# Kernel tuning notes

Measured on AMD Instinct MI355X. Metric: run time of the kernel, lower is better.

The kernel has to match this reference:

```python
import jax, jax.numpy as jnp
import numpy as np
import math

PHI = (1 + math.sqrt(5)) / 2
TABLE_SIZE = 4096
TWO_PI = 2.0 * math.pi
_ang = np.arange(TABLE_SIZE, dtype=np.float32) * (TWO_PI / TABLE_SIZE)
SIN_T = jnp.asarray(np.sin(_ang))
COS_T = jnp.asarray(np.cos(_ang))


def lookup_sin_cos(theta):
    """LUT sin/cos with linear interpolation over a 4096-entry table on [0, 2pi)."""
    pos = (theta / TWO_PI % 1.0) * TABLE_SIZE
    i0f = jnp.floor(pos)
    frac = pos - i0f
    i0 = i0f.astype(jnp.int32) % TABLE_SIZE
    i1 = (i0 + 1) % TABLE_SIZE
    s = SIN_T[i0] * (1.0 - frac) + SIN_T[i1] * frac
    c = COS_T[i0] * (1.0 - frac) + COS_T[i1] * frac
    return s, c


def setup_inputs() -> dict:
    key = jax.random.key(0)
    ks = jax.random.split(key, 8)
    B, S, D, H = 2, 2048, 1024, 16
    dh = D // H
    return {
        "x": jax.random.normal(ks[0], (B, S, D), dtype=jnp.float32),
        "w_q": jax.random.normal(ks[1], (H, dh), dtype=jnp.float32) * 0.02,
        "b_q": jnp.zeros((H, dh), jnp.float32),
        "phi_q": jnp.full((H, dh), PHI, jnp.float32),
        "w_k": jax.random.normal(ks[2], (H, dh), dtype=jnp.float32) * 0.02,
        "b_k": jnp.zeros((H, dh), jnp.float32),
        "phi_k": jnp.full((H, dh), PHI, jnp.float32),
        "w_v": jax.random.normal(ks[3], (H, dh), dtype=jnp.float32) * 0.02,
        "b_v": jnp.zeros((H, dh), jnp.float32),
        "w_out": jax.random.normal(ks[4], (D,), dtype=jnp.float32) * 0.02,
        "b_out": jnp.zeros((D,), jnp.float32),
    }


def reference(x, w_q, b_q, phi_q, w_k, b_k, phi_k, w_v, b_v, w_out, b_out):
    B, S, D = x.shape
    H, dh = w_q.shape
    scale = math.sqrt(2 * dh)
    t = jnp.arange(S, dtype=x.dtype).reshape(1, S, 1, 1)
    xh = x.reshape(B, S, H, dh)

    theta_q = xh / (1.0 + jnp.abs(w_q)) + b_q + t * phi_q
    sin_q, cos_q = lookup_sin_cos(theta_q)
    Q = jnp.concatenate([cos_q, sin_q], axis=-1)  # (B,S,H,2dh)

    theta_k = xh / (1.0 + jnp.abs(w_k)) + b_k + t * phi_k
    sin_k, cos_k = lookup_sin_cos(theta_k)
    K = jnp.concatenate([cos_k, sin_k], axis=-1)  # (B,S,H,2dh)

    theta_v = xh / (1.0 + jnp.abs(w_v)) + b_v
    sin_v, cos_v = lookup_sin_cos(theta_v)
    V = cos_v + sin_v  # (B,S,H,dh)

    scores = jnp.einsum('bqhd,bkhd->bhqk', Q, K) / scale
    causal = jnp.triu(jnp.ones((S, S), dtype=bool), k=1)
    scores = jnp.where(causal, -jnp.inf, scores)
    attn = jax.nn.softmax(scores, axis=-1)
    out = jnp.einsum('bhqk,bkhd->bqhd', attn, V).reshape(B, S, D)

    theta_out = out / (1.0 + jnp.abs(w_out)) + b_out
    sin_o, cos_o = lookup_sin_cos(theta_out)
    return cos_o + sin_o
```

## Files before the change

kernel.cpp:

```cpp
#include <hip/hip_runtime.h>
#include <hip/hip_bf16.h>
#include <math.h>

#define BB 2
#define SS 2048
#define HH 16
#define DH 64
#define DQK 128
#define DD (HH*DH)
#define QS2   0.12751758f
#define EBIAS 11.5415605f

typedef _Float16 half8_t __attribute__((ext_vector_type(8)));
typedef _Float16 half4_t __attribute__((ext_vector_type(4)));
typedef float f32x4_t __attribute__((ext_vector_type(4)));
typedef float f32x4v __attribute__((ext_vector_type(4)));

__device__ __forceinline__ void fsincos(float th, float* sn, float* cs) {
  float rev = th * 0.15915494309189535f;
  rev -= floorf(rev);
#if __has_builtin(__builtin_amdgcn_sinf) && __has_builtin(__builtin_amdgcn_cosf)
  *sn = __builtin_amdgcn_sinf(rev);
  *cs = __builtin_amdgcn_cosf(rev);
#else
  float ang = rev * 6.283185307179586f;
  *sn = __sinf(ang);
  *cs = __cosf(ang);
#endif
}

__device__ __forceinline__ float frcp(float v) {
#if __has_builtin(__builtin_amdgcn_rcpf)
  return __builtin_amdgcn_rcpf(v);
#else
  return 1.f / v;
#endif
}

__device__ __forceinline__ void dma16(const void* g, void* l) {
  __builtin_amdgcn_global_load_lds(
      (const __attribute__((address_space(1))) unsigned int*)g,
      (__attribute__((address_space(3))) unsigned int*)l, 16, 0, 0);
}

__global__ __launch_bounds__(256) void gen_qkv(
    const float* __restrict__ x,
    const float* __restrict__ wq, const float* __restrict__ bq,
    const float* __restrict__ phq,
    const float* __restrict__ wk, const float* __restrict__ bk,
    const float* __restrict__ phk,
    const float* __restrict__ wv, const float* __restrict__ bv,
    _Float16* __restrict__ Qd, _Float16* __restrict__ Kd, _Float16* __restrict__ Vtd)
{
  int stile = blockIdx.x >> 5;
  int bh    = blockIdx.x & 31;
  int b = bh >> 4, h = bh & 15;
  int t = threadIdx.x;
  int sl = t >> 2;
  int dq = (t & 3) << 4;
  int s  = stile * 64 + sl;

  __shared__ _Float16 Vl[64 * 65];

  const float* xr = x + (((size_t)b * SS + s) * HH + h) * DH + dq;
  float tv = (float)s;
  int hd0 = h * DH + dq;
  _Float16 qc[16], qs[16], kc[16], ks[16];
#pragma unroll
  for (int g = 0; g < 4; g++) {
    f32x4v x4  = *(const f32x4v*)(xr + g * 4);
    f32x4v wq4 = *(const f32x4v*)(wq + hd0 + g * 4);
    f32x4v bq4 = *(const f32x4v*)(bq + hd0 + g * 4);
    f32x4v pq4 = *(const f32x4v*)(phq + hd0 + g * 4);
    f32x4v wk4 = *(const f32x4v*)(wk + hd0 + g * 4);
    f32x4v bk4 = *(const f32x4v*)(bk + hd0 + g * 4);
    f32x4v pk4 = *(const f32x4v*)(phk + hd0 + g * 4);
    f32x4v wv4 = *(const f32x4v*)(wv + hd0 + g * 4);
    f32x4v bv4 = *(const f32x4v*)(bv + hd0 + g * 4);
#pragma unroll
    for (int i2 = 0; i2 < 4; i2++) {
      int i = g * 4 + i2;
      float xv = x4[i2];
      {
        float th = xv * frcp(1.f + fabsf(wq4[i2])) + fmaf(tv, pq4[i2], bq4[i2]);
        float sn, cs; fsincos(th, &sn, &cs);
        qc[i] = (_Float16)(cs * QS2);
        qs[i] = (_Float16)(sn * QS2);
      }
      {
        float th = xv * frcp(1.f + fabsf(wk4[i2])) + fmaf(tv, pk4[i2], bk4[i2]);
        float sn, cs; fsincos(th, &sn, &cs);
        kc[i] = (_Float16)cs;
        ks[i] = (_Float16)sn;
      }
      {
        float th = xv * frcp(1.f + fabsf(wv4[i2])) + bv4[i2];
        float sn, cs; fsincos(th, &sn, &cs);
        Vl[(dq + i) * 65 + sl] = (_Float16)(cs + sn);
      }
    }
  }
  size_t qbase = ((size_t)bh * SS + s) * DQK;
#pragma unroll
  for (int i = 0; i < 2; i++) {
    *(half8_t*)(Qd + qbase + dq + i * 8)      = *(half8_t*)(&qc[i * 8]);
    *(half8_t*)(Qd + qbase + DH + dq + i * 8) = *(half8_t*)(&qs[i * 8]);
  }
  {
    size_t ktb = ((size_t)bh * 32 + stile) * 8192;
    int fo0 = (t & 3) * 2;
    *(half8_t*)(Kd + ktb + ((size_t)(fo0    ) * 64 + sl) * 8) = *(half8_t*)(&kc[0]);
    *(half8_t*)(Kd + ktb + ((size_t)(fo0 + 1) * 64 + sl) * 8) = *(half8_t*)(&kc[8]);
    *(half8_t*)(Kd + ktb + ((size_t)(fo0 + 8) * 64 + sl) * 8) = *(half8_t*)(&ks[0]);
    *(half8_t*)(Kd + ktb + ((size_t)(fo0 + 9) * 64 + sl) * 8) = *(half8_t*)(&ks[8]);
  }
  __syncthreads();
#pragma unroll
  for (int i = 0; i < 2; i++) {
    int u = t * 2 + i;
    int dv = u & 63, ku = u >> 6;
    _Float16 tmp[8];
#pragma unroll
    for (int jj = 0; jj < 8; jj++) tmp[jj] = Vl[dv * 65 + ku * 8 + jj];
    *(half8_t*)(Vtd + (((size_t)bh * 32 + stile) * 8 + ku) * 512 + dv * 8) =
        *(half8_t*)tmp;
  }
}

__global__ __launch_bounds__(256) void flash_attn(
    const _Float16* __restrict__ Qd, const _Float16* __restrict__ Kd,
    const _Float16* __restrict__ Vtd,
    const float* __restrict__ wout, const float* __restrict__ bout,
    float* __restrict__ out)
{
  int qt = 31 - (blockIdx.x >> 5);
  int bh = blockIdx.x & 31;
  int b  = bh >> 4, hh = bh & 15;
  int nch = qt + 1;
  int q0 = qt * 64;
  int wave = threadIdx.x >> 6;
  int lane = threadIdx.x & 63;
  int lm = lane & 15, lq = lane >> 4;
  int qh = wave >> 1;
  int kh = wave & 1;

  __shared__ __align__(16) _Float16 KB[2][8192];

  const _Float16* Kg = Kd + (size_t)bh * 32 * 8192;
  const _Float16* Vg = Vtd + (size_t)bh * 32 * 4096;

  {
#pragma unroll
    for (int i = 0; i < 4; i++)
      dma16(Kg + (size_t)(wave * 4 + i) * 512 + lane * 8, &KB[0][(wave * 4 + i) * 512]);
  }

  const _Float16* Qb = Qd + ((size_t)bh * SS + q0 + qh * 32) * DQK;
  half8_t aq[2][4];
#pragma unroll
  for (int qtl = 0; qtl < 2; qtl++)
#pragma unroll
    for (int c = 0; c < 4; c++)
      aq[qtl][c] = *(const half8_t*)(Qb + (qtl * 16 + lm) * DQK + c * 32 + lq * 8);

  f32x4_t o[4][2];
  float l[2] = {0.f, 0.f};
#pragma unroll
  for (int dt = 0; dt < 4; dt++)
#pragma unroll
    for (int qtl = 0; qtl < 2; qtl++) o[dt][qtl] = (f32x4_t){0.f, 0.f, 0.f, 0.f};

  const f32x4_t cinit = (f32x4_t){-EBIAS, -EBIAS, -EBIAS, -EBIAS};

  const _Float16* Vw = Vg + ((size_t)(lq >> 1) * 64 + lm) * 8 + (lq & 1) * 4 +
                       (size_t)kh * 4 * 64 * 8;

  for (int kt = 0; kt < nch; ++kt) {
    int bf = kt & 1;
    __syncthreads();

    half4_t vr[4][2];
    {
      const _Float16* vsrc = Vw + (size_t)kt * 4096;
#pragma unroll
      for (int dt = 0; dt < 4; dt++)
#pragma unroll
        for (int kg = 0; kg < 2; kg++)
          vr[dt][kg] = *(const half4_t*)(vsrc + ((size_t)kg * 2 * 64 + dt * 16) * 8);
    }

    if (kt + 1 < nch) {
      int nb = (kt + 1) & 1;
      const _Float16* gK = Kg + (size_t)(kt + 1) * 8192;
#pragma unroll
      for (int i = 0; i < 4; i++)
        dma16(gK + (size_t)(wave * 4 + i) * 512 + lane * 8, &KB[nb][(wave * 4 + i) * 512]);
    }

    const _Float16* lK = &KB[bf][0];
    int k0 = kt * 64;

    f32x4_t cST[2][2];
    cST[0][0] = cST[0][1] = cST[1][0] = cST[1][1] = cinit;
#pragma unroll
    for (int c = 0; c < 4; c++) {
      half8_t k0f = *(const half8_t*)(lK + ((size_t)(c * 4 + lq) * 64 + kh * 32 + lm) * 8);
      half8_t k1f = *(const half8_t*)(lK + ((size_t)(c * 4 + lq) * 64 + kh * 32 + 16 + lm) * 8);
      cST[0][0] = __builtin_amdgcn_mfma_f32_16x16x32_f16(k0f, aq[0][c], cST[0][0], 0, 0, 0);
      cST[0][1] = __builtin_amdgcn_mfma_f32_16x16x32_f16(k0f, aq[1][c], cST[0][1], 0, 0, 0);
      cST[1][0] = __builtin_amdgcn_mfma_f32_16x16x32_f16(k1f, aq[0][c], cST[1][0], 0, 0, 0);
      cST[1][1] = __builtin_amdgcn_mfma_f32_16x16x32_f16(k1f, aq[1][c], cST[1][1], 0, 0, 0);
    }

    bool maskit = (kt == nch - 1);
    half4_t pb[2][2];
#pragma unroll
    for (int ktl = 0; ktl < 2; ktl++)
#pragma unroll
      for (int qtl = 0; qtl < 2; qtl++) {
        float pf[4];
#pragma unroll
        for (int r = 0; r < 4; r++) {
          float sv = cST[ktl][qtl][r];
          if (maskit) {
            int key  = k0 + kh * 32 + ktl * 16 + lq * 4 + r;
            int qrow = q0 + qh * 32 + qtl * 16 + lm;
            if (key > qrow) sv = -1e30f;
          }
          pf[r] = __builtin_exp2f(sv);
          l[qtl] += pf[r];
        }
        pb[ktl][qtl] = (half4_t){(_Float16)pf[0], (_Float16)pf[1],
                                 (_Float16)pf[2], (_Float16)pf[3]};
      }

#pragma unroll
    for (int dt = 0; dt < 4; dt++)
#pragma unroll
      for (int kg = 0; kg < 2; kg++) {
        o[dt][0] = __builtin_amdgcn_mfma_f32_16x16x16f16(vr[dt][kg], pb[kg][0], o[dt][0], 0, 0, 0);
        o[dt][1] = __builtin_amdgcn_mfma_f32_16x16x16f16(vr[dt][kg], pb[kg][1], o[dt][1], 0, 0, 0);
      }
  }

#pragma unroll
  for (int qtl = 0; qtl < 2; qtl++) {
    l[qtl] += __shfl_xor(l[qtl], 16);
    l[qtl] += __shfl_xor(l[qtl], 32);
  }

  float* Of = (float*)&KB[0][0];
  float* Lf = Of + 64 * 68;
  __syncthreads();
  if (kh == 1) {
#pragma unroll
    for (int qtl = 0; qtl < 2; qtl++) {
      int row = qh * 32 + qtl * 16 + lm;
#pragma unroll
      for (int dt = 0; dt < 4; dt++)
#pragma unroll
        for (int r = 0; r < 4; r++)
          Of[row * 68 + dt * 16 + lq * 4 + r] = o[dt][qtl][r];
      if (lq == 0) Lf[row] = l[qtl];
    }
  }
  __syncthreads();
  if (kh == 0) {
#pragma unroll
    for (int qtl = 0; qtl < 2; qtl++) {
      int row = qh * 32 + qtl * 16 + lm;
      float rl = frcp(l[qtl] + Lf[row]);
#pragma unroll
      for (int dt = 0; dt < 4; dt++)
#pragma unroll
        for (int r = 0; r < 4; r++) {
          int idx = row * 68 + dt * 16 + lq * 4 + r;
          Of[idx] = (o[dt][qtl][r] + Of[idx]) * rl;
        }
    }
  }
  __syncthreads();
  {
    int dcol = hh * DH + lane;
    float iw = frcp(1.f + fabsf(wout[dcol]));
    float bo = bout[dcol];
#pragma unroll
    for (int rr = 0; rr < 16; rr++) {
      int row = wave * 16 + rr;
      float th = Of[row * 68 + lane] * iw + bo;
      float sn, cs; fsincos(th, &sn, &cs);
      out[((size_t)b * SS + q0 + row) * DD + dcol] = cs + sn;
    }
  }
}

extern "C" void kernel_launch(void* const* d_in, const int* in_sizes, int n_in,
                              void* d_out, int out_size, void* d_ws, size_t ws_size,
                              hipStream_t stream) {
  (void)in_sizes; (void)n_in; (void)out_size; (void)ws_size;
  const float* x   = (const float*)d_in[0];
  const float* wq  = (const float*)d_in[1];
  const float* bq  = (const float*)d_in[2];
  const float* phq = (const float*)d_in[3];
  const float* wk  = (const float*)d_in[4];
  const float* bk  = (const float*)d_in[5];
  const float* phk = (const float*)d_in[6];
  const float* wv  = (const float*)d_in[7];
  const float* bv  = (const float*)d_in[8];
  const float* wo  = (const float*)d_in[9];
  const float* bo  = (const float*)d_in[10];

  _Float16* Qd  = (_Float16*)d_ws;
  _Float16* Kd  = Qd + (size_t)BB * HH * SS * DQK;
  _Float16* Vtd = Kd + (size_t)BB * HH * SS * DQK;

  gen_qkv<<<BB * HH * (SS / 64), 256, 0, stream>>>(
      x, wq, bq, phq, wk, bk, phk, wv, bv, Qd, Kd, Vtd);
  flash_attn<<<32 * 32, 256, 0, stream>>>(
      Qd, Kd, Vtd, wo, bo, (float*)d_out);
}
```

Baseline: 141.6 us.

## Load K tiles directly from global into registers, drop LDS double buffering

Removes the double-buffered LDS staging of K, which used global_load_lds DMA and a barrier every iteration. Each wave now loads its K fragments straight from global memory into registers, as V already was. This removes the per-iteration __syncthreads and frees LDS, which may raise occupancy. In exchange, K reuse across the two waves that share a key half now relies on the caches, and there is no explicit prefetch of the next tile.

```diff
diff --git a/kernel.cpp b/kernel.cpp
--- a/kernel.cpp
+++ b/kernel.cpp
@@ -35,12 +35,6 @@
 #else
   return 1.f / v;
 #endif
-}
-
-__device__ __forceinline__ void dma16(const void* g, void* l) {
-  __builtin_amdgcn_global_load_lds(
-      (const __attribute__((address_space(1))) unsigned int*)g,
-      (__attribute__((address_space(3))) unsigned int*)l, 16, 0, 0);
 }
 
 __global__ __launch_bounds__(256) void gen_qkv(
@@ -144,16 +138,13 @@
   int qh = wave >> 1;
   int kh = wave & 1;
 
-  __shared__ __align__(16) _Float16 KB[2][8192];
+  __shared__ __align__(16) float Of[64 * 68];
+  __shared__ __align__(16) float Lf[64];
 
   const _Float16* Kg = Kd + (size_t)bh * 32 * 8192;
-  const _Float16* Vg = Vtd + (size_t)bh * 32 * 4096;
-
-  {
-#pragma unroll
-    for (int i = 0; i < 4; i++)
-      dma16(Kg + (size_t)(wave * 4 + i) * 512 + lane * 8, &KB[0][(wave * 4 + i) * 512]);
-  }
+  const _Float16* Kw = Kg + ((size_t)lq * 64 + kh * 32 + lm) * 8;
+  const _Float16* Vw = Vtd + (size_t)bh * 32 * 4096 +
+                       ((size_t)(kh * 4 + (lq >> 1)) * 64 + lm) * 8 + (lq & 1) * 4;
 
   const _Float16* Qb = Qd + ((size_t)bh * SS + q0 + qh * 32) * DQK;
   half8_t aq[2][4];
@@ -172,44 +163,32 @@
 
   const f32x4_t cinit = (f32x4_t){-EBIAS, -EBIAS, -EBIAS, -EBIAS};
 
-  const _Float16* Vw = Vg + ((size_t)(lq >> 1) * 64 + lm) * 8 + (lq & 1) * 4 +
-                       (size_t)kh * 4 * 64 * 8;
-
   for (int kt = 0; kt < nch; ++kt) {
-    int bf = kt & 1;
-    __syncthreads();
-
+    const _Float16* Kc = Kw + (size_t)kt * 8192;
+    const _Float16* Vc = Vw + (size_t)kt * 4096;
+    int k0 = kt * 64;
+
+    half8_t kf[2][4];
+#pragma unroll
+    for (int c = 0; c < 4; c++) {
+      kf[0][c] = *(const half8_t*)(Kc + (size_t)c * 4 * 64 * 8);
+      kf[1][c] = *(const half8_t*)(Kc + (size_t)c * 4 * 64 * 8 + 16 * 8);
+    }
     half4_t vr[4][2];
-    {
-      const _Float16* vsrc = Vw + (size_t)kt * 4096;
-#pragma unroll
-      for (int dt = 0; dt < 4; dt++)
-#pragma unroll
-        for (int kg = 0; kg < 2; kg++)
-          vr[dt][kg] = *(const half4_t*)(vsrc + ((size_t)kg * 2 * 64 + dt * 16) * 8);
-    }
-
-    if (kt + 1 < nch) {
-      int nb = (kt + 1) & 1;
-      const _Float16* gK = Kg + (size_t)(kt + 1) * 8192;
-#pragma unroll
-      for (int i = 0; i < 4; i++)
-        dma16(gK + (size_t)(wave * 4 + i) * 512 + lane * 8, &KB[nb][(wave * 4 + i) * 512]);
-    }
-
-    const _Float16* lK = &KB[bf][0];
-    int k0 = kt * 64;
+#pragma unroll
+    for (int dt = 0; dt < 4; dt++)
+#pragma unroll
+      for (int kg = 0; kg < 2; kg++)
+        vr[dt][kg] = *(const half4_t*)(Vc + ((size_t)kg * 2 * 64 + dt * 16) * 8);
 
     f32x4_t cST[2][2];
     cST[0][0] = cST[0][1] = cST[1][0] = cST[1][1] = cinit;
 #pragma unroll
     for (int c = 0; c < 4; c++) {
-      half8_t k0f = *(const half8_t*)(lK + ((size_t)(c * 4 + lq) * 64 + kh * 32 + lm) * 8);
-      half8_t k1f = *(const half8_t*)(lK + ((size_t)(c * 4 + lq) * 64 + kh * 32 + 16 + lm) * 8);
-      cST[0][0] = __builtin_amdgcn_mfma_f32_16x16x32_f16(k0f, aq[0][c], cST[0][0], 0, 0, 0);
-      cST[0][1] = __builtin_amdgcn_mfma_f32_16x16x32_f16(k0f, aq[1][c], cST[0][1], 0, 0, 0);
-      cST[1][0] = __builtin_amdgcn_mfma_f32_16x16x32_f16(k1f, aq[0][c], cST[1][0], 0, 0, 0);
-      cST[1][1] = __builtin_amdgcn_mfma_f32_16x16x32_f16(k1f, aq[1][c], cST[1][1], 0, 0, 0);
+      cST[0][0] = __builtin_amdgcn_mfma_f32_16x16x32_f16(kf[0][c], aq[0][c], cST[0][0], 0, 0, 0);
+      cST[0][1] = __builtin_amdgcn_mfma_f32_16x16x32_f16(kf[0][c], aq[1][c], cST[0][1], 0, 0, 0);
+      cST[1][0] = __builtin_amdgcn_mfma_f32_16x16x32_f16(kf[1][c], aq[0][c], cST[1][0], 0, 0, 0);
+      cST[1][1] = __builtin_amdgcn_mfma_f32_16x16x32_f16(kf[1][c], aq[1][c], cST[1][1], 0, 0, 0);
     }
 
     bool maskit = (kt == nch - 1);
@@ -249,9 +228,6 @@
     l[qtl] += __shfl_xor(l[qtl], 32);
   }
 
-  float* Of = (float*)&KB[0][0];
-  float* Lf = Of + 64 * 68;
-  __syncthreads();
   if (kh == 1) {
 #pragma unroll
     for (int qtl = 0; qtl < 2; qtl++) {
```

Result: slower. 148.0 us (+4.5%).

## Use 128-row query tiles with 8 waves and stage V through shared memory

Applied to the files above, without the earlier changes.

Flash attention blocks now cover 128 query rows with 512 threads (8 waves), so each K/V chunk loaded into shared memory is reused by twice as many queries and the grid halves. V tiles are now DMA'd into LDS alongside K and double-buffered, instead of being read per-lane straight from global memory. Waves whose query rows lie entirely above a key chunk skip its compute, and the causal mask applies per wave. Block scheduling is reordered to pair long and short causal tiles. The cost is more LDS per block and fewer resident blocks, and the reduction buffer now needs 128 rows of scratch inside the enlarged KV array.

```diff
diff --git a/kernel.cpp b/kernel.cpp
--- a/kernel.cpp
+++ b/kernel.cpp
@@ -127,32 +127,34 @@
   }
 }
 
-__global__ __launch_bounds__(256) void flash_attn(
+__global__ __launch_bounds__(512) void flash_attn(
     const _Float16* __restrict__ Qd, const _Float16* __restrict__ Kd,
     const _Float16* __restrict__ Vtd,
     const float* __restrict__ wout, const float* __restrict__ bout,
     float* __restrict__ out)
 {
-  int qt = 31 - (blockIdx.x >> 5);
+  int o_ = blockIdx.x >> 5;
+  int qt = (o_ < 8) ? (15 - o_) : (o_ - 8);
   int bh = blockIdx.x & 31;
   int b  = bh >> 4, hh = bh & 15;
-  int nch = qt + 1;
-  int q0 = qt * 64;
+  int nch = 2 * qt + 2;
+  int q0 = qt * 128;
   int wave = threadIdx.x >> 6;
   int lane = threadIdx.x & 63;
   int lm = lane & 15, lq = lane >> 4;
   int qh = wave >> 1;
   int kh = wave & 1;
 
-  __shared__ __align__(16) _Float16 KB[2][8192];
+  __shared__ __align__(16) _Float16 KV[2][12288];
 
   const _Float16* Kg = Kd + (size_t)bh * 32 * 8192;
   const _Float16* Vg = Vtd + (size_t)bh * 32 * 4096;
 
   {
 #pragma unroll
-    for (int i = 0; i < 4; i++)
-      dma16(Kg + (size_t)(wave * 4 + i) * 512 + lane * 8, &KB[0][(wave * 4 + i) * 512]);
+    for (int i = 0; i < 2; i++)
+      dma16(Kg + (size_t)(wave * 2 + i) * 512 + lane * 8, &KV[0][(wave * 2 + i) * 512]);
+    dma16(Vg + (size_t)wave * 512 + lane * 8, &KV[0][8192 + wave * 512]);
   }
 
   const _Float16* Qb = Qd + ((size_t)bh * SS + q0 + qh * 32) * DQK;
@@ -171,34 +173,26 @@
     for (int qtl = 0; qtl < 2; qtl++) o[dt][qtl] = (f32x4_t){0.f, 0.f, 0.f, 0.f};
 
   const f32x4_t cinit = (f32x4_t){-EBIAS, -EBIAS, -EBIAS, -EBIAS};
-
-  const _Float16* Vw = Vg + ((size_t)(lq >> 1) * 64 + lm) * 8 + (lq & 1) * 4 +
-                       (size_t)kh * 4 * 64 * 8;
+  int qtop = q0 + qh * 32;
 
   for (int kt = 0; kt < nch; ++kt) {
     int bf = kt & 1;
     __syncthreads();
-
-    half4_t vr[4][2];
-    {
-      const _Float16* vsrc = Vw + (size_t)kt * 4096;
-#pragma unroll
-      for (int dt = 0; dt < 4; dt++)
-#pragma unroll
-        for (int kg = 0; kg < 2; kg++)
-          vr[dt][kg] = *(const half4_t*)(vsrc + ((size_t)kg * 2 * 64 + dt * 16) * 8);
-    }
-
     if (kt + 1 < nch) {
       int nb = (kt + 1) & 1;
       const _Float16* gK = Kg + (size_t)(kt + 1) * 8192;
-#pragma unroll
-      for (int i = 0; i < 4; i++)
-        dma16(gK + (size_t)(wave * 4 + i) * 512 + lane * 8, &KB[nb][(wave * 4 + i) * 512]);
-    }
-
-    const _Float16* lK = &KB[bf][0];
+      const _Float16* gV = Vg + (size_t)(kt + 1) * 4096;
+#pragma unroll
+      for (int i = 0; i < 2; i++)
+        dma16(gK + (size_t)(wave * 2 + i) * 512 + lane * 8, &KV[nb][(wave * 2 + i) * 512]);
+      dma16(gV + (size_t)wave * 512 + lane * 8, &KV[nb][8192 + wave * 512]);
+    }
+
     int k0 = kt * 64;
+    if (k0 > qtop + 31) continue;
+
+    const _Float16* lK = &KV[bf][0];
+    const _Float16* lV = &KV[bf][8192];
 
     f32x4_t cST[2][2];
     cST[0][0] = cST[0][1] = cST[1][0] = cST[1][1] = cinit;
@@ -212,7 +206,7 @@
       cST[1][1] = __builtin_amdgcn_mfma_f32_16x16x32_f16(k1f, aq[1][c], cST[1][1], 0, 0, 0);
     }
 
-    bool maskit = (kt == nch - 1);
+    bool maskit = (k0 + 63 > qtop);
     half4_t pb[2][2];
 #pragma unroll
     for (int ktl = 0; ktl < 2; ktl++)
@@ -224,7 +218,7 @@
           float sv = cST[ktl][qtl][r];
           if (maskit) {
             int key  = k0 + kh * 32 + ktl * 16 + lq * 4 + r;
-            int qrow = q0 + qh * 32 + qtl * 16 + lm;
+            int qrow = qtop + qtl * 16 + lm;
             if (key > qrow) sv = -1e30f;
           }
           pf[r] = __builtin_exp2f(sv);
@@ -238,8 +232,10 @@
     for (int dt = 0; dt < 4; dt++)
 #pragma unroll
       for (int kg = 0; kg < 2; kg++) {
-        o[dt][0] = __builtin_amdgcn_mfma_f32_16x16x16f16(vr[dt][kg], pb[kg][0], o[dt][0], 0, 0, 0);
-        o[dt][1] = __builtin_amdgcn_mfma_f32_16x16x16f16(vr[dt][kg], pb[kg][1], o[dt][1], 0, 0, 0);
+        half4_t vf = *(const half4_t*)(lV +
+            ((size_t)(kh * 4 + kg * 2 + (lq >> 1)) * 64 + dt * 16 + lm) * 8 + (lq & 1) * 4);
+        o[dt][0] = __builtin_amdgcn_mfma_f32_16x16x16f16(vf, pb[kg][0], o[dt][0], 0, 0, 0);
+        o[dt][1] = __builtin_amdgcn_mfma_f32_16x16x16f16(vf, pb[kg][1], o[dt][1], 0, 0, 0);
       }
   }
 
@@ -249,8 +245,8 @@
     l[qtl] += __shfl_xor(l[qtl], 32);
   }
 
-  float* Of = (float*)&KB[0][0];
-  float* Lf = Of + 64 * 68;
+  float* Of = (float*)&KV[0][0];
+  float* Lf = Of + 128 * 68;
   __syncthreads();
   if (kh == 1) {
 #pragma unroll
@@ -316,6 +312,6 @@
 
   gen_qkv<<<BB * HH * (SS / 64), 256, 0, stream>>>(
       x, wq, bq, phq, wk, bk, phk, wv, bv, Qd, Kd, Vtd);
-  flash_attn<<<32 * 32, 256, 0, stream>>>(
+  flash_attn<<<16 * 32, 512, 0, stream>>>(
       Qd, Kd, Vtd, wo, bo, (float*)d_out);
 }
```

Result: slower. 150.2 us (+6.0%).
